# Optimization experiments

Hardware: AMD Instinct MI355X
Metric: run time of the kernel (lower is better)

## Reference

```python
import jax, jax.numpy as jnp
import numpy as np

B, T, F = 32, 4096, 512
H = 512

def setup_inputs() -> dict:
    key = jax.random.key(0)
    k1, k2, k3, k4, k5 = jax.random.split(key, 5)
    enc = jax.random.normal(k1, (B, T, F), dtype=jnp.float32)
    dec = jax.random.normal(k2, (B, F), dtype=jnp.float32)
    # Dense kernels (no bias), scaled like Glorot-ish init
    W1 = jax.random.normal(k3, (F, H), dtype=jnp.float32) / np.sqrt(F)
    W2 = jax.random.normal(k4, (F, H), dtype=jnp.float32) / np.sqrt(F)
    V = jax.random.normal(k5, (H, 1), dtype=jnp.float32) / np.sqrt(H)
    return {"encoder_outputs": enc, "dec_output": dec, "W1": W1, "W2": W2, "V": V}

def reference(encoder_outputs, dec_output, W1, W2, V):
    # Bahdanau additive attention, fully vectorized over time_steps
    # (the original runs this step-by-step via K.rnn; state is unchanged,
    # so the computation is embarrassingly parallel over t).
    w1_e = jnp.einsum('btf,fh->bth', encoder_outputs, W1)   # [B,T,H]
    w2_d = jnp.einsum('bf,fh->bh', dec_output, W2)          # [B,H]
    scores = jnp.einsum('bth,h->bt', jnp.tanh(w1_e + w2_d[:, None, :]), V[:, 0])  # [B,T]
    return jax.nn.softmax(scores, axis=1)
```

## Files before the change

kernel.cpp:

```cpp
#include <hip/hip_runtime.h>
#include <hip/hip_bf16.h>

#define B_ 32
#define T_ 4096
#define F_ 512
#define H_ 512

typedef float floatx4 __attribute__((ext_vector_type(4)));
typedef short short8 __attribute__((ext_vector_type(8)));

__device__ __forceinline__ unsigned pack2_bf16(float a, float b) {
  unsigned ua = __float_as_uint(a);
  unsigned ub = __float_as_uint(b);
  ua = (ua + 0x7FFFu + ((ua >> 16) & 1u)) >> 16;
  ub = (ub + 0x7FFFu + ((ub >> 16) & 1u)) & 0xFFFF0000u;
  return ua | ub;
}

__device__ __forceinline__ unsigned short f2bf16(float a) {
  unsigned ua = __float_as_uint(a);
  return (unsigned short)((ua + 0x7FFFu + ((ua >> 16) & 1u)) >> 16);
}

__device__ __forceinline__ float tanh_fast(float x) {
  float e = __expf(2.0f * x);
  return 1.0f - __fdividef(2.0f, e + 1.0f);
}

__device__ __forceinline__ void async_load16(const void* g, void* l) {
  __builtin_amdgcn_global_load_lds(
      (const __attribute__((address_space(1))) void*)g,
      (__attribute__((address_space(3))) void*)l, 16, 0, 0);
}

__global__ void prep_w1t(const float* __restrict__ W1, unsigned short* __restrict__ W1T) {
  __shared__ float tile[32][33];
  const int tx = threadIdx.x, ty = threadIdx.y;
  const int f = blockIdx.y * 32 + ty;
  const int h = blockIdx.x * 32 + tx;
  tile[ty][tx] = W1[f * H_ + h];
  __syncthreads();
  const int ho = blockIdx.x * 32 + ty;
  const int fo = blockIdx.y * 32 + tx;
  W1T[ho * F_ + fo] = f2bf16(tile[tx][ty]);
}

__global__ __launch_bounds__(128) void prep_w2d(const float* __restrict__ dec,
                                                const float* __restrict__ W2,
                                                float* __restrict__ w2d) {
  const int b = blockIdx.x;
  const int h = blockIdx.y * 128 + threadIdx.x;
  float s0 = 0.f, s1 = 0.f, s2 = 0.f, s3 = 0.f;
  for (int f = 0; f < F_; f += 4) {
    s0 += dec[b * F_ + f + 0] * W2[(f + 0) * H_ + h];
    s1 += dec[b * F_ + f + 1] * W2[(f + 1) * H_ + h];
    s2 += dec[b * F_ + f + 2] * W2[(f + 2) * H_ + h];
    s3 += dec[b * F_ + f + 3] * W2[(f + 3) * H_ + h];
  }
  w2d[b * H_ + h] = (s0 + s1) + (s2 + s3);
}

__global__ __launch_bounds__(256, 3) void fused_score(
    const float* __restrict__ enc, const unsigned short* __restrict__ W1T,
    const float* __restrict__ w2d, const float* __restrict__ V,
    float* __restrict__ scores) {
  __shared__ __align__(16) unsigned short As[2][128 * 40];
  __shared__ __align__(16) unsigned short Bs[2][128 * 32];

  const int tid = threadIdx.x;
  const int bid = blockIdx.x;
  const int xcd = bid & 7;
  const int ii = bid >> 3;
  const int n_blk = ii & 3;
  const int m_blk = xcd + ((ii >> 2) << 3);
  const int lane = tid & 63;
  const int wave = tid >> 6;
  const int wm = wave >> 1;
  const int wn = wave & 1;
  const int quad = lane >> 4;
  const int l16 = lane & 15;

  const int arow = tid >> 2;
  const int acol = (tid & 3) * 8;
  const float* aptr = enc + (size_t)(m_blk * 128 + arow) * F_ + acol;

  const int nb0 = wave * 32;
  const int bl_n = lane >> 2;
  const int bl_c = (lane & 3) ^ (bl_n & 3);
  const unsigned short* bsrc0 =
      W1T + (size_t)(n_blk * 128 + nb0 + bl_n) * F_ + bl_c * 8;
  const unsigned short* bsrc1 = bsrc0 + 16 * F_;

  floatx4 acc[4][4];
#pragma unroll
  for (int i = 0; i < 4; i++)
#pragma unroll
    for (int j = 0; j < 4; j++) acc[i][j] = (floatx4){0.f, 0.f, 0.f, 0.f};

  float4 a_pre[4];

#pragma unroll
  for (int rr = 0; rr < 2; ++rr) {
    a_pre[rr * 2 + 0] = *(const float4*)(aptr + rr * 64 * F_ + 0);
    a_pre[rr * 2 + 1] = *(const float4*)(aptr + rr * 64 * F_ + 4);
  }
#pragma unroll
  for (int rr = 0; rr < 2; ++rr) {
    uint4 pk;
    pk.x = pack2_bf16(a_pre[rr * 2].x, a_pre[rr * 2].y);
    pk.y = pack2_bf16(a_pre[rr * 2].z, a_pre[rr * 2].w);
    pk.z = pack2_bf16(a_pre[rr * 2 + 1].x, a_pre[rr * 2 + 1].y);
    pk.w = pack2_bf16(a_pre[rr * 2 + 1].z, a_pre[rr * 2 + 1].w);
    *(uint4*)&As[0][(arow + rr * 64) * 40 + acol] = pk;
  }
  async_load16(bsrc0, &Bs[0][nb0 * 32]);
  async_load16(bsrc1, &Bs[0][(nb0 + 16) * 32]);
  __syncthreads();

  for (int ks = 0; ks < 16; ++ks) {
    const int cur = ks & 1;
    const int nxt = cur ^ 1;

    if (ks < 15) {
      const int k1 = (ks + 1) * 32;
#pragma unroll
      for (int rr = 0; rr < 2; ++rr) {
        a_pre[rr * 2 + 0] = *(const float4*)(aptr + rr * 64 * F_ + k1);
        a_pre[rr * 2 + 1] = *(const float4*)(aptr + rr * 64 * F_ + k1 + 4);
      }
      async_load16(bsrc0 + k1, &Bs[nxt][nb0 * 32]);
      async_load16(bsrc1 + k1, &Bs[nxt][(nb0 + 16) * 32]);
    }

    short8 af[4], bfr[4];
#pragma unroll
    for (int i = 0; i < 4; i++)
      af[i] = *(const short8*)&As[cur][(wm * 64 + i * 16 + l16) * 40 + quad * 8];
#pragma unroll
    for (int j = 0; j < 4; j++)
      bfr[j] = *(const short8*)&Bs[cur][(wn * 64 + j * 16 + l16) * 32 +
                                        ((quad ^ (l16 & 3)) * 8)];
#pragma unroll
    for (int i = 0; i < 4; i++)
#pragma unroll
      for (int j = 0; j < 4; j++)
        acc[i][j] = __builtin_amdgcn_mfma_f32_16x16x32_bf16(af[i], bfr[j], acc[i][j], 0, 0, 0);

    if (ks < 15) {
#pragma unroll
      for (int rr = 0; rr < 2; ++rr) {
        uint4 pk;
        pk.x = pack2_bf16(a_pre[rr * 2].x, a_pre[rr * 2].y);
        pk.y = pack2_bf16(a_pre[rr * 2].z, a_pre[rr * 2].w);
        pk.z = pack2_bf16(a_pre[rr * 2 + 1].x, a_pre[rr * 2 + 1].y);
        pk.w = pack2_bf16(a_pre[rr * 2 + 1].z, a_pre[rr * 2 + 1].w);
        *(uint4*)&As[nxt][(arow + rr * 64) * 40 + acol] = pk;
      }
    }
    __syncthreads();
  }

  const int b = m_blk >> 5;
  float w2v[4], vv[4];
#pragma unroll
  for (int j = 0; j < 4; j++) {
    const int h = n_blk * 128 + wn * 64 + j * 16 + l16;
    w2v[j] = w2d[b * H_ + h];
    vv[j] = V[h];
  }
  float rs[4][4];
#pragma unroll
  for (int i = 0; i < 4; i++)
#pragma unroll
    for (int r = 0; r < 4; r++) {
      float s = 0.f;
#pragma unroll
      for (int j = 0; j < 4; j++) s += tanh_fast(acc[i][j][r] + w2v[j]) * vv[j];
      rs[i][r] = s;
    }
#pragma unroll
  for (int i = 0; i < 4; i++)
#pragma unroll
    for (int r = 0; r < 4; r++) {
      float s = rs[i][r];
      s += __shfl_xor(s, 1, 16);
      s += __shfl_xor(s, 2, 16);
      s += __shfl_xor(s, 4, 16);
      s += __shfl_xor(s, 8, 16);
      rs[i][r] = s;
    }
  if (l16 == 0) {
#pragma unroll
    for (int i = 0; i < 4; i++)
#pragma unroll
      for (int r = 0; r < 4; r++)
        atomicAdd(&scores[m_blk * 128 + wm * 64 + i * 16 + quad * 4 + r], rs[i][r]);
  }
}

__global__ __launch_bounds__(256) void softmax_rows(const float* __restrict__ scores,
                                                    float* __restrict__ out) {
  const int b = blockIdx.x;
  const int tid = threadIdx.x;
  const int wave = tid >> 6;
  __shared__ float red[4];
  float v[16];
  float mx = -1e30f;
#pragma unroll
  for (int i = 0; i < 16; i++) {
    v[i] = scores[b * T_ + i * 256 + tid];
    mx = fmaxf(mx, v[i]);
  }
#pragma unroll
  for (int o = 32; o > 0; o >>= 1) mx = fmaxf(mx, __shfl_xor(mx, o, 64));
  if ((tid & 63) == 0) red[wave] = mx;
  __syncthreads();
  mx = fmaxf(fmaxf(red[0], red[1]), fmaxf(red[2], red[3]));
  __syncthreads();
  float sum = 0.f;
#pragma unroll
  for (int i = 0; i < 16; i++) {
    v[i] = __expf(v[i] - mx);
    sum += v[i];
  }
#pragma unroll
  for (int o = 32; o > 0; o >>= 1) sum += __shfl_xor(sum, o, 64);
  if ((tid & 63) == 0) red[wave] = sum;
  __syncthreads();
  sum = (red[0] + red[1]) + (red[2] + red[3]);
  const float inv = 1.0f / sum;
#pragma unroll
  for (int i = 0; i < 16; i++) out[b * T_ + i * 256 + tid] = v[i] * inv;
}

extern "C" void kernel_launch(void* const* d_in, const int* in_sizes, int n_in,
                              void* d_out, int out_size, void* d_ws, size_t ws_size,
                              hipStream_t stream) {
  const float* enc = (const float*)d_in[0];
  const float* dec = (const float*)d_in[1];
  const float* W1 = (const float*)d_in[2];
  const float* W2 = (const float*)d_in[3];
  const float* V = (const float*)d_in[4];
  float* out = (float*)d_out;

  char* ws = (char*)d_ws;
  float* scores = (float*)ws;
  unsigned short* W1T = (unsigned short*)(ws + 524288);
  float* w2d = (float*)(ws + 1048576);

  (void)in_sizes; (void)n_in; (void)out_size; (void)ws_size;

  hipMemsetAsync(scores, 0, B_ * T_ * sizeof(float), stream);
  prep_w1t<<<dim3(16, 16), dim3(32, 32), 0, stream>>>(W1, W1T);
  prep_w2d<<<dim3(32, 4), dim3(128), 0, stream>>>(dec, W2, w2d);
  fused_score<<<dim3(4096), dim3(256), 0, stream>>>(enc, W1T, w2d, V, scores);
  softmax_rows<<<dim3(32), dim3(256), 0, stream>>>(scores, out);
}
```

Before: 477.2 us.

## Merge prep kernels, use intrinsic bf16 conversion, raise fused_score occupancy hint

Combines the W1 transpose and the dec·W2 projection into one prep launch, which removes one kernel launch. The manual round-to-nearest bf16 packing is replaced by __float2bfloat16, which the compiler may lower to hardware conversion instructions. The launch_bounds minimum-blocks hint for the main GEMM kernel is raised from 3 to 4, trading register budget for occupancy and risking spills. The async LDS load helper is simply inlined.

```diff
diff --git a/kernel.cpp b/kernel.cpp
--- a/kernel.cpp
+++ b/kernel.cpp
@@ -9,14 +9,6 @@
 typedef float floatx4 __attribute__((ext_vector_type(4)));
 typedef short short8 __attribute__((ext_vector_type(8)));
 
-__device__ __forceinline__ unsigned pack2_bf16(float a, float b) {
-  unsigned ua = __float_as_uint(a);
-  unsigned ub = __float_as_uint(b);
-  ua = (ua + 0x7FFFu + ((ua >> 16) & 1u)) >> 16;
-  ub = (ub + 0x7FFFu + ((ub >> 16) & 1u)) & 0xFFFF0000u;
-  return ua | ub;
-}
-
 __device__ __forceinline__ unsigned short f2bf16(float a) {
   unsigned ua = __float_as_uint(a);
   return (unsigned short)((ua + 0x7FFFu + ((ua >> 16) & 1u)) >> 16);
@@ -27,40 +19,51 @@
   return 1.0f - __fdividef(2.0f, e + 1.0f);
 }
 
-__device__ __forceinline__ void async_load16(const void* g, void* l) {
-  __builtin_amdgcn_global_load_lds(
-      (const __attribute__((address_space(1))) void*)g,
-      (__attribute__((address_space(3))) void*)l, 16, 0, 0);
-}
-
-__global__ void prep_w1t(const float* __restrict__ W1, unsigned short* __restrict__ W1T) {
+__device__ __forceinline__ short8 cvt8(float4 lo, float4 hi) {
+  union { short8 s8; __hip_bfloat16 h[8]; } u;
+  u.h[0] = __float2bfloat16(lo.x);
+  u.h[1] = __float2bfloat16(lo.y);
+  u.h[2] = __float2bfloat16(lo.z);
+  u.h[3] = __float2bfloat16(lo.w);
+  u.h[4] = __float2bfloat16(hi.x);
+  u.h[5] = __float2bfloat16(hi.y);
+  u.h[6] = __float2bfloat16(hi.z);
+  u.h[7] = __float2bfloat16(hi.w);
+  return u.s8;
+}
+
+__global__ __launch_bounds__(1024) void prep_all(const float* __restrict__ W1,
+                                                 unsigned short* __restrict__ W1T,
+                                                 const float* __restrict__ dec,
+                                                 const float* __restrict__ W2,
+                                                 float* __restrict__ w2d) {
   __shared__ float tile[32][33];
-  const int tx = threadIdx.x, ty = threadIdx.y;
-  const int f = blockIdx.y * 32 + ty;
-  const int h = blockIdx.x * 32 + tx;
-  tile[ty][tx] = W1[f * H_ + h];
-  __syncthreads();
-  const int ho = blockIdx.x * 32 + ty;
-  const int fo = blockIdx.y * 32 + tx;
-  W1T[ho * F_ + fo] = f2bf16(tile[tx][ty]);
-}
-
-__global__ __launch_bounds__(128) void prep_w2d(const float* __restrict__ dec,
-                                                const float* __restrict__ W2,
-                                                float* __restrict__ w2d) {
-  const int b = blockIdx.x;
-  const int h = blockIdx.y * 128 + threadIdx.x;
-  float s0 = 0.f, s1 = 0.f, s2 = 0.f, s3 = 0.f;
-  for (int f = 0; f < F_; f += 4) {
-    s0 += dec[b * F_ + f + 0] * W2[(f + 0) * H_ + h];
-    s1 += dec[b * F_ + f + 1] * W2[(f + 1) * H_ + h];
-    s2 += dec[b * F_ + f + 2] * W2[(f + 2) * H_ + h];
-    s3 += dec[b * F_ + f + 3] * W2[(f + 3) * H_ + h];
-  }
-  w2d[b * H_ + h] = (s0 + s1) + (s2 + s3);
-}
-
-__global__ __launch_bounds__(256, 3) void fused_score(
+  if (blockIdx.x < 256) {
+    const int tx = threadIdx.x & 31, ty = threadIdx.x >> 5;
+    const int bx = blockIdx.x & 15, by = blockIdx.x >> 4;
+    const int f = by * 32 + ty;
+    const int h = bx * 32 + tx;
+    tile[ty][tx] = W1[f * H_ + h];
+    __syncthreads();
+    const int ho = bx * 32 + ty;
+    const int fo = by * 32 + tx;
+    W1T[ho * F_ + fo] = f2bf16(tile[tx][ty]);
+  } else {
+    const int g = (blockIdx.x - 256) * 1024 + threadIdx.x;
+    const int b = g >> 9;
+    const int h = g & 511;
+    float s0 = 0.f, s1 = 0.f, s2 = 0.f, s3 = 0.f;
+    for (int f = 0; f < F_; f += 4) {
+      s0 += dec[b * F_ + f + 0] * W2[(f + 0) * H_ + h];
+      s1 += dec[b * F_ + f + 1] * W2[(f + 1) * H_ + h];
+      s2 += dec[b * F_ + f + 2] * W2[(f + 2) * H_ + h];
+      s3 += dec[b * F_ + f + 3] * W2[(f + 3) * H_ + h];
+    }
+    w2d[b * H_ + h] = (s0 + s1) + (s2 + s3);
+  }
+}
+
+__global__ __launch_bounds__(256, 4) void fused_score(
     const float* __restrict__ enc, const unsigned short* __restrict__ W1T,
     const float* __restrict__ w2d, const float* __restrict__ V,
     float* __restrict__ scores) {
@@ -106,15 +109,17 @@
   }
 #pragma unroll
   for (int rr = 0; rr < 2; ++rr) {
-    uint4 pk;
-    pk.x = pack2_bf16(a_pre[rr * 2].x, a_pre[rr * 2].y);
-    pk.y = pack2_bf16(a_pre[rr * 2].z, a_pre[rr * 2].w);
-    pk.z = pack2_bf16(a_pre[rr * 2 + 1].x, a_pre[rr * 2 + 1].y);
-    pk.w = pack2_bf16(a_pre[rr * 2 + 1].z, a_pre[rr * 2 + 1].w);
-    *(uint4*)&As[0][(arow + rr * 64) * 40 + acol] = pk;
-  }
-  async_load16(bsrc0, &Bs[0][nb0 * 32]);
-  async_load16(bsrc1, &Bs[0][(nb0 + 16) * 32]);
+    short8 pk = cvt8(a_pre[rr * 2 + 0], a_pre[rr * 2 + 1]);
+    *(short8*)&As[0][(arow + rr * 64) * 40 + acol] = pk;
+  }
+  {
+    __builtin_amdgcn_global_load_lds(
+        (const __attribute__((address_space(1))) void*)bsrc0,
+        (__attribute__((address_space(3))) void*)&Bs[0][nb0 * 32], 16, 0, 0);
+    __builtin_amdgcn_global_load_lds(
+        (const __attribute__((address_space(1))) void*)bsrc1,
+        (__attribute__((address_space(3))) void*)&Bs[0][(nb0 + 16) * 32], 16, 0, 0);
+  }
   __syncthreads();
 
   for (int ks = 0; ks < 16; ++ks) {
@@ -128,8 +133,12 @@
         a_pre[rr * 2 + 0] = *(const float4*)(aptr + rr * 64 * F_ + k1);
         a_pre[rr * 2 + 1] = *(const float4*)(aptr + rr * 64 * F_ + k1 + 4);
       }
-      async_load16(bsrc0 + k1, &Bs[nxt][nb0 * 32]);
-      async_load16(bsrc1 + k1, &Bs[nxt][(nb0 + 16) * 32]);
+      __builtin_amdgcn_global_load_lds(
+          (const __attribute__((address_space(1))) void*)(bsrc0 + k1),
+          (__attribute__((address_space(3))) void*)&Bs[nxt][nb0 * 32], 16, 0, 0);
+      __builtin_amdgcn_global_load_lds(
+          (const __attribute__((address_space(1))) void*)(bsrc1 + k1),
+          (__attribute__((address_space(3))) void*)&Bs[nxt][(nb0 + 16) * 32], 16, 0, 0);
     }
 
     short8 af[4], bfr[4];
@@ -149,12 +158,8 @@
     if (ks < 15) {
 #pragma unroll
       for (int rr = 0; rr < 2; ++rr) {
-        uint4 pk;
-        pk.x = pack2_bf16(a_pre[rr * 2].x, a_pre[rr * 2].y);
-        pk.y = pack2_bf16(a_pre[rr * 2].z, a_pre[rr * 2].w);
-        pk.z = pack2_bf16(a_pre[rr * 2 + 1].x, a_pre[rr * 2 + 1].y);
-        pk.w = pack2_bf16(a_pre[rr * 2 + 1].z, a_pre[rr * 2 + 1].w);
-        *(uint4*)&As[nxt][(arow + rr * 64) * 40 + acol] = pk;
+        short8 pk = cvt8(a_pre[rr * 2 + 0], a_pre[rr * 2 + 1]);
+        *(short8*)&As[nxt][(arow + rr * 64) * 40 + acol] = pk;
       }
     }
     __syncthreads();
@@ -251,8 +256,7 @@
   (void)in_sizes; (void)n_in; (void)out_size; (void)ws_size;
 
   hipMemsetAsync(scores, 0, B_ * T_ * sizeof(float), stream);
-  prep_w1t<<<dim3(16, 16), dim3(32, 32), 0, stream>>>(W1, W1T);
-  prep_w2d<<<dim3(32, 4), dim3(128), 0, stream>>>(dec, W2, w2d);
+  prep_all<<<dim3(272), dim3(1024), 0, stream>>>(W1, W1T, dec, W2, w2d);
   fused_score<<<dim3(4096), dim3(256), 0, stream>>>(enc, W1T, w2d, V, scores);
   softmax_rows<<<dim3(32), dim3(256), 0, stream>>>(scores, out);
 }
```

Result: no change. 478.2 us (+0.2%).
